# Performance work log

Hardware: AMD Instinct MI355X
Metric: run time of the kernel (lower is better)

Reference implementation:

```python
import jax, jax.numpy as jnp
import numpy as np

B, D, N, K = 16, 128, 4096, 1024


def setup_inputs() -> dict:
    key = jax.random.key(0)
    k1, k2 = jax.random.split(key)
    ze = jax.random.normal(k1, (B, D, N), dtype=jnp.float32)
    emb = jax.random.normal(k2, (K, D), dtype=jnp.float32)
    return {"ze": ze, "emb": emb}


def reference(ze, emb):
    """VQ forward: nearest-codebook quantization with straight-through estimator.

    ze:  (B, D, N) encoder latents (D = n_latent_dim, N = timesteps)
    emb: (K, D) codebook (stop-gradient applied, matching StopGrad on emb)
    returns zq_rg: (B, D, N) quantized latents; gradient flows straight to ze
    (ReplaceGrad: zq gets zero grad, ze gets the output grad).
    """
    emb_sg = jax.lax.stop_gradient(emb)
    # Squared L2 distance via expansion, avoiding the (B, D, K, N) broadcast:
    # d2[b,k,n] = ||ze[b,:,n]||^2 + ||emb[k]||^2 - 2 <ze[b,:,n], emb[k]>
    ze_sq = jnp.sum(ze * ze, axis=1)            # (B, N)
    emb_sq = jnp.sum(emb_sg * emb_sg, axis=1)   # (K,)
    dot = jnp.einsum('bdn,kd->bkn', ze, emb_sg)  # (B, K, N)
    d2 = ze_sq[:, None, :] + emb_sq[None, :, None] - 2.0 * dot
    ind = jnp.argmin(d2, axis=1)                # (B, N) nearest codebook index
    zq = jnp.transpose(jnp.take(emb_sg, ind, axis=0), (0, 2, 1))  # (B, D, N)
    # ReplaceGrad straight-through: value of zq, gradient routed to ze.
    zq_rg = ze + jax.lax.stop_gradient(zq - ze)
    return zq_rg
```

## Files before the change

### kernel.cpp

```cpp
#include <hip/hip_runtime.h>
#include <hip/hip_bf16.h>
#include <math.h>

#define BB 16
#define DD 128
#define NN 4096
#define KK 1024
#define CADD 320.0f
#define TAU 0.45f

typedef __attribute__((ext_vector_type(8))) short short8;
typedef __attribute__((ext_vector_type(4))) float f32x4;

static __device__ __forceinline__ unsigned short f32_bf16_rne(float f) {
    unsigned u = __float_as_uint(f);
    u += 0x7FFF + ((u >> 16) & 1);
    return (unsigned short)(u >> 16);
}
static __device__ __forceinline__ unsigned umin32(unsigned a, unsigned b) { return a < b ? a : b; }
static __device__ __forceinline__ unsigned umax32(unsigned a, unsigned b) { return a > b ? a : b; }
static __device__ __forceinline__ unsigned umed3(unsigned a, unsigned b, unsigned c) {
    unsigned d;
    asm("v_med3_u32 %0, %1, %2, %3" : "=v"(d) : "v"(a), "v"(b), "v"(c));
    return d;
}

__global__ void emb_sq_kernel(const float* __restrict__ emb,
                              float* __restrict__ e2) {
    int k = blockIdx.x * 256 + threadIdx.x;
    if (k >= KK) return;
    const float4* row = reinterpret_cast<const float4*>(emb + (size_t)k * DD);
    float a0 = 0.f, a1 = 0.f, a2 = 0.f, a3 = 0.f;
#pragma unroll
    for (int i = 0; i < DD / 16; ++i) {
        float4 v0 = row[i * 4 + 0];
        float4 v1 = row[i * 4 + 1];
        float4 v2 = row[i * 4 + 2];
        float4 v3 = row[i * 4 + 3];
        a0 += v0.x * v0.x + v0.y * v0.y + v0.z * v0.z + v0.w * v0.w;
        a1 += v1.x * v1.x + v1.y * v1.y + v1.z * v1.z + v1.w * v1.w;
        a2 += v2.x * v2.x + v2.y * v2.y + v2.z * v2.z + v2.w * v2.w;
        a3 += v3.x * v3.x + v3.y * v3.y + v3.z * v3.z + v3.w * v3.w;
    }
    e2[k] = (a0 + a1) + (a2 + a3) + CADD;
}

__global__ void emb_pack_kernel(const float* __restrict__ emb,
                                short* __restrict__ epk) {
    int g = blockIdx.x * 256 + threadIdx.x;
    int lane = g & 63;
    int s    = (g >> 6) & 3;
    int t    = g >> 8;
    int k = t * 16 + (lane & 15);
    int d = s * 32 + ((lane >> 4) & 3) * 8;
    const float* src = emb + (size_t)k * DD + d;
    short8 h;
#pragma unroll
    for (int j = 0; j < 8; ++j) h[j] = (short)f32_bf16_rne(-2.0f * src[j]);
    *reinterpret_cast<short8*>(epk + (size_t)g * 8) = h;
}

#define CEU(a, b) { unsigned lo_ = umin32(a, b), hi_ = umax32(a, b); (a) = lo_; (b) = hi_; }
#define MRG9(A1, A2, A3, A4, B1, B2, B3, B4) \
    CEU(A1, B1) CEU(A2, B2) CEU(A3, B3) CEU(A4, B4) \
    CEU(A3, B1) CEU(A4, B2) \
    CEU(A2, A3) \
    CEU(A4, B1) \
    CEU(A3, A4)

__global__ __launch_bounds__(256, 4)
void vq_mfma(const float* __restrict__ ze, const float* __restrict__ emb,
             const short* __restrict__ epk, const float* __restrict__ e2,
             float* __restrict__ out) {
    __shared__ __align__(16) char ubuf[(DD + 1) * 32 * 4];
    __shared__ unsigned kbuf[4][32][4];
    __shared__ int winner_s[32];
    __shared__ int rlist[32];
    __shared__ int rcnt;

    short* zstage = reinterpret_cast<short*>(ubuf);

    const int tid  = threadIdx.x;
    const int lane = tid & 63;
    const int wave = tid >> 6;
    const int b    = blockIdx.x >> 7;
    const int n0b  = (blockIdx.x & 127) * 32;
    const float* zb = ze + (size_t)b * DD * NN;

    const int nq = lane & 15;
    const int dq = (lane >> 4) & 3;

#pragma unroll
    for (int cg = 0; cg < 2; ++cg) {
        const int col = n0b + cg * 16 + nq;
        const int d0  = wave * 32 + dq * 8;
        const float* zp = zb + (size_t)d0 * NN + col;
        short8 h;
#pragma unroll
        for (int j = 0; j < 8; ++j) h[j] = (short)f32_bf16_rne(zp[(size_t)j * NN]);
        *reinterpret_cast<short8*>(zstage + (cg * 256 + wave * 64 + lane) * 8) = h;
    }
    __syncthreads();

    short8 zf[2][4];
#pragma unroll
    for (int cg = 0; cg < 2; ++cg)
#pragma unroll
        for (int s = 0; s < 4; ++s)
            zf[cg][s] = *reinterpret_cast<const short8*>(
                zstage + ((cg * 4 + s) * 64 + lane) * 8);
    __syncthreads();

    unsigned K1[2], K2[2];
    K1[0] = K1[1] = K2[0] = K2[1] = 0xFFFFFFFFu;

    const int t0 = wave * 16;
    const short* ep  = epk + (size_t)(t0 * 4) * 512 + (size_t)lane * 8;
    const float* e2p = e2 + t0 * 16 + dq * 4;
    unsigned kb = (unsigned)(t0 * 16 + dq * 4);

    short8 aC0 = *reinterpret_cast<const short8*>(ep);
    short8 aC1 = *reinterpret_cast<const short8*>(ep + 512);
    short8 aC2 = *reinterpret_cast<const short8*>(ep + 1024);
    short8 aC3 = *reinterpret_cast<const short8*>(ep + 1536);
    float4 evC = *reinterpret_cast<const float4*>(e2p);

#pragma unroll 2
    for (int tt = 0; tt < 16; ++tt) {
        short8 aN0, aN1, aN2, aN3; float4 evN;
        if (tt < 15) {
            aN0 = *reinterpret_cast<const short8*>(ep + 2048);
            aN1 = *reinterpret_cast<const short8*>(ep + 2560);
            aN2 = *reinterpret_cast<const short8*>(ep + 3072);
            aN3 = *reinterpret_cast<const short8*>(ep + 3584);
            evN = *reinterpret_cast<const float4*>(e2p + 16);
            asm volatile("s_waitcnt vmcnt(5)" ::: "memory");
        } else {
            asm volatile("s_waitcnt vmcnt(0)" ::: "memory");
        }
        __builtin_amdgcn_sched_barrier(0);

        f32x4 acc0 = {evC.x, evC.y, evC.z, evC.w};
        f32x4 acc1 = acc0;
#define STEP(AF, S) \
        acc0 = __builtin_amdgcn_mfma_f32_16x16x32_bf16(AF, zf[0][S], acc0, 0, 0, 0); \
        acc1 = __builtin_amdgcn_mfma_f32_16x16x32_bf16(AF, zf[1][S], acc1, 0, 0, 0);
        STEP(aC0, 0) STEP(aC1, 1) STEP(aC2, 2) STEP(aC3, 3)
#undef STEP

#pragma unroll
        for (int cg = 0; cg < 2; ++cg) {
            const f32x4 a = (cg == 0) ? acc0 : acc1;
#pragma unroll
            for (int r = 0; r < 4; ++r) {
                const unsigned x = (__float_as_uint(a[r]) & 0xFFFFFC00u) | (kb + r);
                K2[cg] = umed3(K1[cg], K2[cg], x);
                K1[cg] = umin32(K1[cg], x);
            }
        }
        kb += 16; ep += 2048; e2p += 16;
        aC0 = aN0; aC1 = aN1; aC2 = aN2; aC3 = aN3; evC = evN;
    }

    unsigned T1[2], T2[2], T3[2], T4[2];
#pragma unroll
    for (int cg = 0; cg < 2; ++cg) {
        unsigned A1 = K1[cg], A2 = K2[cg];
        unsigned B1 = __shfl_xor(A1, 16);
        unsigned B2 = __shfl_xor(A2, 16);
        CEU(A1, B1) CEU(A2, B2) CEU(A2, B1)
        unsigned C1 = __shfl_xor(A1, 32);
        unsigned C2 = __shfl_xor(A2, 32);
        unsigned C3 = __shfl_xor(B1, 32);
        unsigned C4 = __shfl_xor(B2, 32);
        MRG9(A1, A2, B1, B2, C1, C2, C3, C4)
        T1[cg] = A1; T2[cg] = A2; T3[cg] = B1; T4[cg] = B2;
    }

    if (lane < 32) {
        const int cgid = lane >> 4;
        kbuf[wave][lane][0] = cgid ? T1[1] : T1[0];
        kbuf[wave][lane][1] = cgid ? T2[1] : T2[0];
        kbuf[wave][lane][2] = cgid ? T3[1] : T3[0];
        kbuf[wave][lane][3] = cgid ? T4[1] : T4[0];
    }
    __syncthreads();

    if (wave == 0) {
        const int c = lane & 31;
        unsigned A1 = kbuf[0][c][0], A2 = kbuf[0][c][1];
        unsigned A3 = kbuf[0][c][2], A4 = kbuf[0][c][3];
#pragma unroll
        for (int q = 1; q < 4; ++q) {
            unsigned B1 = kbuf[q][c][0], B2 = kbuf[q][c][1];
            unsigned B3 = kbuf[q][c][2], B4 = kbuf[q][c][3];
            MRG9(A1, A2, A3, A4, B1, B2, B3, B4)
        }
        const float M1 = __uint_as_float(A1 & 0xFFFFFC00u);
        const float M2 = __uint_as_float(A2 & 0xFFFFFC00u);
        const bool trig = (lane < 32) && ((M2 - M1) < TAU);
        if (lane < 32) {
            winner_s[c] = (int)(A1 & 0x3FFu);
            kbuf[0][c][0] = A1; kbuf[0][c][1] = A2;
            kbuf[0][c][2] = A3; kbuf[0][c][3] = A4;
        }
        const unsigned long long mask = __ballot(trig);
        if (trig) {
            const int idx = __popcll(mask & ((1ull << lane) - 1ull));
            rlist[idx] = c;
        }
        if (lane == 0) rcnt = (int)__popcll(mask);
    }
    __syncthreads();

    {
        const int rc = rcnt;
        for (int j = wave; j < rc; j += 4) {
            const int c = rlist[j];
            const int coln = n0b + c;
            const int I0 = (int)(kbuf[0][c][0] & 0x3FFu);
            const int I1 = (int)(kbuf[0][c][1] & 0x3FFu);
            const int I2 = (int)(kbuf[0][c][2] & 0x3FFu);
            const int I3 = (int)(kbuf[0][c][3] & 0x3FFu);
            double s0 = 0.0, s1 = 0.0, s2 = 0.0, s3 = 0.0;
#pragma unroll
            for (int h = 0; h < 2; ++h) {
                const int d = h * 64 + lane;
                const double zv = (double)zb[(size_t)d * NN + coln];
                double q;
                q = zv - (double)emb[(size_t)I0 * DD + d]; s0 += q * q;
                q = zv - (double)emb[(size_t)I1 * DD + d]; s1 += q * q;
                q = zv - (double)emb[(size_t)I2 * DD + d]; s2 += q * q;
                q = zv - (double)emb[(size_t)I3 * DD + d]; s3 += q * q;
            }
#pragma unroll
            for (int off = 1; off < 64; off <<= 1) {
                s0 += __shfl_xor(s0, off);
                s1 += __shfl_xor(s1, off);
                s2 += __shfl_xor(s2, off);
                s3 += __shfl_xor(s3, off);
            }
            int best = I0; double db = s0;
            if (s1 < db || (s1 == db && I1 < best)) { db = s1; best = I1; }
            if (s2 < db || (s2 == db && I2 < best)) { db = s2; best = I2; }
            if (s3 < db || (s3 == db && I3 < best)) { db = s3; best = I3; }
            if (lane == 0) winner_s[c] = best;
        }
    }
    __syncthreads();

    float (*ew)[DD + 1] = reinterpret_cast<float(*)[DD + 1]>(ubuf);
#pragma unroll 2
    for (int rr = 0; rr < 8; ++rr) {
        const int r = wave * 8 + rr;
        const int idx = winner_s[r];
        ew[r][lane]      = emb[(size_t)idx * DD + lane];
        ew[r][lane + 64] = emb[(size_t)idx * DD + lane + 64];
    }
    __syncthreads();

    {
        const int c = lane & 31;
        const int coln = n0b + c;
#pragma unroll 4
        for (int dd = 0; dd < 16; ++dd) {
            const int d = wave * 32 + dd * 2 + (lane >> 5);
            const float zv = zb[(size_t)d * NN + coln];
            const float evv = ew[c][d];
            out[((size_t)b * DD + d) * NN + coln] = zv + (evv - zv);
        }
    }
}

extern "C" void kernel_launch(void* const* d_in, const int* in_sizes, int n_in,
                              void* d_out, int out_size, void* d_ws, size_t ws_size,
                              hipStream_t stream) {
    (void)in_sizes; (void)n_in; (void)out_size; (void)ws_size;
    const float* ze  = (const float*)d_in[0];
    const float* emb = (const float*)d_in[1];
    float*       out = (float*)d_out;

    char* ws = (char*)d_ws;
    short* epk = (short*)ws;
    float* e2  = (float*)(ws + (size_t)KK * DD * 2);

    emb_sq_kernel<<<KK / 256, 256, 0, stream>>>(emb, e2);
    emb_pack_kernel<<<(KK * DD / 8) / 256, 256, 0, stream>>>(emb, epk);
    vq_mfma<<<(BB * NN) / 32, 256, 0, stream>>>(ze, emb, epk, e2, out);
}
```

Baseline: 49.72 us.

## Triple-buffer codebook fragment loads and stage emb norms in LDS

Deepens the codebook prefetch pipeline from double to triple buffering, issuing loads two iterations ahead with adjusted vmcnt waits, and fully unrolls the 16-iteration loop. The per-tile codebook squared norms are copied into shared memory once per block and read from LDS instead of global memory inside the loop. This is meant to hide global load latency behind the MFMA work. In exchange it uses more registers and adds LDS traffic, which could lower occupancy.

Result: faster. 47.37 us (-4.7%).

```diff
diff --git a/kernel.cpp b/kernel.cpp
--- a/kernel.cpp
+++ b/kernel.cpp
@@ -90,6 +90,8 @@
     const int nq = lane & 15;
     const int dq = (lane >> 4) & 3;
 
+    float* e2w = reinterpret_cast<float*>(ubuf + 8192) + wave * 256;
+
 #pragma unroll
     for (int cg = 0; cg < 2; ++cg) {
         const int col = n0b + cg * 16 + nq;
@@ -100,6 +102,9 @@
         for (int j = 0; j < 8; ++j) h[j] = (short)f32_bf16_rne(zp[(size_t)j * NN]);
         *reinterpret_cast<short8*>(zstage + (cg * 256 + wave * 64 + lane) * 8) = h;
     }
+#pragma unroll
+    for (int i = 0; i < 4; ++i)
+        e2w[i * 64 + lane] = e2[wave * 256 + i * 64 + lane];
     __syncthreads();
 
     short8 zf[2][4];
@@ -115,37 +120,46 @@
     K1[0] = K1[1] = K2[0] = K2[1] = 0xFFFFFFFFu;
 
     const int t0 = wave * 16;
-    const short* ep  = epk + (size_t)(t0 * 4) * 512 + (size_t)lane * 8;
-    const float* e2p = e2 + t0 * 16 + dq * 4;
+    const short* ep = epk + (size_t)(t0 * 4) * 512 + (size_t)lane * 8;
     unsigned kb = (unsigned)(t0 * 16 + dq * 4);
 
-    short8 aC0 = *reinterpret_cast<const short8*>(ep);
-    short8 aC1 = *reinterpret_cast<const short8*>(ep + 512);
-    short8 aC2 = *reinterpret_cast<const short8*>(ep + 1024);
-    short8 aC3 = *reinterpret_cast<const short8*>(ep + 1536);
-    float4 evC = *reinterpret_cast<const float4*>(e2p);
-
-#pragma unroll 2
+    short8 Af[3][4];
+#pragma unroll
+    for (int s = 0; s < 4; ++s)
+        Af[0][s] = *reinterpret_cast<const short8*>(ep + s * 512);
+#pragma unroll
+    for (int s = 0; s < 4; ++s)
+        Af[1][s] = *reinterpret_cast<const short8*>(ep + 2048 + s * 512);
+
+    float4 evC = *reinterpret_cast<const float4*>(e2w + dq * 4);
+
+#pragma unroll
     for (int tt = 0; tt < 16; ++tt) {
-        short8 aN0, aN1, aN2, aN3; float4 evN;
-        if (tt < 15) {
-            aN0 = *reinterpret_cast<const short8*>(ep + 2048);
-            aN1 = *reinterpret_cast<const short8*>(ep + 2560);
-            aN2 = *reinterpret_cast<const short8*>(ep + 3072);
-            aN3 = *reinterpret_cast<const short8*>(ep + 3584);
-            evN = *reinterpret_cast<const float4*>(e2p + 16);
-            asm volatile("s_waitcnt vmcnt(5)" ::: "memory");
+        const int cur = tt % 3;
+        if (tt < 14) {
+            const int nxt = (tt + 2) % 3;
+            const short* epn = ep + (size_t)(tt + 2) * 2048;
+#pragma unroll
+            for (int s = 0; s < 4; ++s)
+                Af[nxt][s] = *reinterpret_cast<const short8*>(epn + s * 512);
+            asm volatile("s_waitcnt vmcnt(8)" ::: "memory");
+        } else if (tt == 14) {
+            asm volatile("s_waitcnt vmcnt(4)" ::: "memory");
         } else {
             asm volatile("s_waitcnt vmcnt(0)" ::: "memory");
         }
         __builtin_amdgcn_sched_barrier(0);
+
+        const float4 evN = (tt < 15)
+            ? *reinterpret_cast<const float4*>(e2w + (tt + 1) * 16 + dq * 4)
+            : evC;
 
         f32x4 acc0 = {evC.x, evC.y, evC.z, evC.w};
         f32x4 acc1 = acc0;
 #define STEP(AF, S) \
         acc0 = __builtin_amdgcn_mfma_f32_16x16x32_bf16(AF, zf[0][S], acc0, 0, 0, 0); \
         acc1 = __builtin_amdgcn_mfma_f32_16x16x32_bf16(AF, zf[1][S], acc1, 0, 0, 0);
-        STEP(aC0, 0) STEP(aC1, 1) STEP(aC2, 2) STEP(aC3, 3)
+        STEP(Af[cur][0], 0) STEP(Af[cur][1], 1) STEP(Af[cur][2], 2) STEP(Af[cur][3], 3)
 #undef STEP
 
 #pragma unroll
@@ -158,8 +172,8 @@
                 K1[cg] = umin32(K1[cg], x);
             }
         }
-        kb += 16; ep += 2048; e2p += 16;
-        aC0 = aN0; aC1 = aN1; aC2 = aN2; aC3 = aN3; evC = evN;
+        kb += 16;
+        evC = evN;
     }
 
     unsigned T1[2], T2[2], T3[2], T4[2];
```

## Stream codebook tiles via global_load_lds double buffer and cache e2 in LDS

Applied to the files above, without the earlier changes.

Codebook bf16 tiles are now fetched with direct global-to-LDS loads into a per-wave double buffer, replacing register prefetch. This is meant to cut VGPR pressure and the vmcnt-gated register copies. The squared codebook norms are staged once into LDS per block. The z fragments are now loaded straight into registers by every wave, so the shared-memory staging pass and its two barriers go away. The cost is four times the global/L2 reads for z and a larger LDS footprint per block, which could limit occupancy.

Measured after the change: 55.33 us. +11.3%, slower.

```diff
diff --git a/kernel.cpp b/kernel.cpp
--- a/kernel.cpp
+++ b/kernel.cpp
@@ -11,6 +11,9 @@
 
 typedef __attribute__((ext_vector_type(8))) short short8;
 typedef __attribute__((ext_vector_type(4))) float f32x4;
+
+typedef __attribute__((address_space(3))) char       lds_char;
+typedef __attribute__((address_space(1))) const char gbl_char;
 
 static __device__ __forceinline__ unsigned short f32_bf16_rne(float f) {
     unsigned u = __float_as_uint(f);
@@ -72,13 +75,12 @@
 void vq_mfma(const float* __restrict__ ze, const float* __restrict__ emb,
              const short* __restrict__ epk, const float* __restrict__ e2,
              float* __restrict__ out) {
-    __shared__ __align__(16) char ubuf[(DD + 1) * 32 * 4];
+    __shared__ __align__(16) char stg[32768];
+    __shared__ float e2l[KK];
     __shared__ unsigned kbuf[4][32][4];
     __shared__ int winner_s[32];
     __shared__ int rlist[32];
     __shared__ int rcnt;
-
-    short* zstage = reinterpret_cast<short*>(ubuf);
 
     const int tid  = threadIdx.x;
     const int lane = tid & 63;
@@ -90,63 +92,68 @@
     const int nq = lane & 15;
     const int dq = (lane >> 4) & 3;
 
+    float* e2w = e2l + wave * 256;
+#pragma unroll
+    for (int i = 0; i < 4; ++i)
+        e2w[i * 64 + lane] = e2[wave * 256 + i * 64 + lane];
+
+    short8 zf[2][4];
 #pragma unroll
     for (int cg = 0; cg < 2; ++cg) {
         const int col = n0b + cg * 16 + nq;
-        const int d0  = wave * 32 + dq * 8;
-        const float* zp = zb + (size_t)d0 * NN + col;
-        short8 h;
-#pragma unroll
-        for (int j = 0; j < 8; ++j) h[j] = (short)f32_bf16_rne(zp[(size_t)j * NN]);
-        *reinterpret_cast<short8*>(zstage + (cg * 256 + wave * 64 + lane) * 8) = h;
-    }
-    __syncthreads();
-
-    short8 zf[2][4];
-#pragma unroll
-    for (int cg = 0; cg < 2; ++cg)
-#pragma unroll
-        for (int s = 0; s < 4; ++s)
-            zf[cg][s] = *reinterpret_cast<const short8*>(
-                zstage + ((cg * 4 + s) * 64 + lane) * 8);
-    __syncthreads();
+#pragma unroll
+        for (int s = 0; s < 4; ++s) {
+            const float* zp = zb + (size_t)(s * 32 + dq * 8) * NN + col;
+#pragma unroll
+            for (int j = 0; j < 8; ++j)
+                zf[cg][s][j] = (short)f32_bf16_rne(zp[(size_t)j * NN]);
+        }
+    }
 
     unsigned K1[2], K2[2];
     K1[0] = K1[1] = K2[0] = K2[1] = 0xFFFFFFFFu;
 
     const int t0 = wave * 16;
-    const short* ep  = epk + (size_t)(t0 * 4) * 512 + (size_t)lane * 8;
-    const float* e2p = e2 + t0 * 16 + dq * 4;
+    const short* ep_l = epk + (size_t)(t0 * 4) * 512 + (size_t)lane * 8;
+    char* stw = stg + wave * 8192;
+
+    auto issue_tile = [&](int tt) {
+        char* lb = stw + (tt & 1) * 4096;
+        const short* gs = ep_l + (size_t)tt * 2048;
+#pragma unroll
+        for (int s = 0; s < 4; ++s) {
+            __builtin_amdgcn_global_load_lds(
+                (gbl_char*)(gs + s * 512),
+                (lds_char*)(lb + s * 1024), 16, 0, 0);
+        }
+    };
+
+    asm volatile("s_waitcnt vmcnt(0)" ::: "memory");
+    issue_tile(0);
+
     unsigned kb = (unsigned)(t0 * 16 + dq * 4);
-
-    short8 aC0 = *reinterpret_cast<const short8*>(ep);
-    short8 aC1 = *reinterpret_cast<const short8*>(ep + 512);
-    short8 aC2 = *reinterpret_cast<const short8*>(ep + 1024);
-    short8 aC3 = *reinterpret_cast<const short8*>(ep + 1536);
-    float4 evC = *reinterpret_cast<const float4*>(e2p);
+    const int lro = lane * 16;
 
 #pragma unroll 2
     for (int tt = 0; tt < 16; ++tt) {
-        short8 aN0, aN1, aN2, aN3; float4 evN;
         if (tt < 15) {
-            aN0 = *reinterpret_cast<const short8*>(ep + 2048);
-            aN1 = *reinterpret_cast<const short8*>(ep + 2560);
-            aN2 = *reinterpret_cast<const short8*>(ep + 3072);
-            aN3 = *reinterpret_cast<const short8*>(ep + 3584);
-            evN = *reinterpret_cast<const float4*>(e2p + 16);
-            asm volatile("s_waitcnt vmcnt(5)" ::: "memory");
+            issue_tile(tt + 1);
+            asm volatile("s_waitcnt vmcnt(4)" ::: "memory");
         } else {
             asm volatile("s_waitcnt vmcnt(0)" ::: "memory");
         }
         __builtin_amdgcn_sched_barrier(0);
 
-        f32x4 acc0 = {evC.x, evC.y, evC.z, evC.w};
+        const char* lb = stw + (tt & 1) * 4096;
+        const float4 ev = *reinterpret_cast<const float4*>(e2w + tt * 16 + dq * 4);
+        f32x4 acc0 = {ev.x, ev.y, ev.z, ev.w};
         f32x4 acc1 = acc0;
-#define STEP(AF, S) \
-        acc0 = __builtin_amdgcn_mfma_f32_16x16x32_bf16(AF, zf[0][S], acc0, 0, 0, 0); \
-        acc1 = __builtin_amdgcn_mfma_f32_16x16x32_bf16(AF, zf[1][S], acc1, 0, 0, 0);
-        STEP(aC0, 0) STEP(aC1, 1) STEP(aC2, 2) STEP(aC3, 3)
-#undef STEP
+#pragma unroll
+        for (int s = 0; s < 4; ++s) {
+            const short8 af = *reinterpret_cast<const short8*>(lb + s * 1024 + lro);
+            acc0 = __builtin_amdgcn_mfma_f32_16x16x32_bf16(af, zf[0][s], acc0, 0, 0, 0);
+            acc1 = __builtin_amdgcn_mfma_f32_16x16x32_bf16(af, zf[1][s], acc1, 0, 0, 0);
+        }
 
 #pragma unroll
         for (int cg = 0; cg < 2; ++cg) {
@@ -158,8 +165,7 @@
                 K1[cg] = umin32(K1[cg], x);
             }
         }
-        kb += 16; ep += 2048; e2p += 16;
-        aC0 = aN0; aC1 = aN1; aC2 = aN2; aC3 = aN3; evC = evN;
+        kb += 16;
     }
 
     unsigned T1[2], T2[2], T3[2], T4[2];
@@ -249,7 +255,7 @@
     }
     __syncthreads();
 
-    float (*ew)[DD + 1] = reinterpret_cast<float(*)[DD + 1]>(ubuf);
+    float (*ew)[DD + 1] = reinterpret_cast<float(*)[DD + 1]>(stg);
 #pragma unroll 2
     for (int rr = 0; rr < 8; ++rr) {
         const int r = wave * 8 + rr;
```
